# Kernel tuning notes

Measured on AMD Instinct MI355X. Metric: run time of the kernel, lower is better.

The kernel has to match this reference:

```python
import jax, jax.numpy as jnp
import numpy as np

B, N, D, C, H = 32, 36, 2048, 4, 512  # batch, regions, feat dim, coord dim, fusion hidden


def setup_inputs() -> dict:
    key = jax.random.key(0)
    ks = jax.random.split(key, 8)
    w = lambda k, sh: jax.random.normal(k, sh, dtype=jnp.float32) * 0.02
    return {
        "mm": jax.random.normal(ks[0], (B, N, D), dtype=jnp.float32),
        "coords": jax.random.uniform(ks[1], (B, N, C), dtype=jnp.float32),
        # MLB fusion params for coords: z = (x@W_cl * y@W_cr) @ W_cout
        "W_cl": w(ks[2], (C, H)),
        "W_cr": w(ks[3], (C, H)),
        "W_cout": w(ks[4], (H, D)),
        # MLB fusion params for features
        "W_fl": w(ks[5], (D, H)),
        "W_fr": w(ks[6], (D, H)),
        "W_fout": w(ks[7], (H, D)),
    }


def reference(mm, coords, W_cl, W_cr, W_cout, W_fl, W_fr, W_fout):
    # Project once per region (avoids projecting inside the N*N expand).
    cl = coords @ W_cl            # [B,N,H]
    cr = coords @ W_cr            # [B,N,H]
    fl = mm @ W_fl                # [B,N,H]
    fr = mm @ W_fr                # [B,N,H]
    # All-pairs bilinear fusion: Rij = f_coord(c_i, c_j) + f_feat(m_i, m_j)
    pair_c = cl[:, :, None, :] * cr[:, None, :, :]   # [B,N,N,H]
    pair_f = fl[:, :, None, :] * fr[:, None, :, :]   # [B,N,N,H]
    Rij = (jnp.einsum('bijh,hd->bijd', pair_c, W_cout)
           + jnp.einsum('bijh,hd->bijd', pair_f, W_fout))  # [B,N,N,D]
    # agg['type'] == 'max': reduce over the right (j) region axis
    mm_new = Rij.max(axis=2)      # [B,N,D]
    # residual
    return mm_new + mm
```

## Files before the change

### kernel.cpp

```cpp
#include <hip/hip_runtime.h>


typedef __attribute__((ext_vector_type(8))) short short8;
typedef __attribute__((ext_vector_type(4))) short short4v;
typedef __attribute__((ext_vector_type(4))) float f32x4;

__device__ __forceinline__ float bf2f(unsigned short h) {
  return __uint_as_float(((unsigned int)h) << 16);
}
__device__ __forceinline__ unsigned short f2bf(float f) {
  unsigned int u = __float_as_uint(f);
  u += 0x7FFFu + ((u >> 16) & 1u);
  return (unsigned short)(u >> 16);
}
__device__ __forceinline__ void gl2lds16(const void* g, void* l) {
  __builtin_amdgcn_global_load_lds(
      (const __attribute__((address_space(1))) unsigned int*)g,
      (__attribute__((address_space(3))) unsigned int*)l, 16, 0, 0);
}

__global__ __launch_bounds__(256) void k_prep(
    const float* __restrict__ coords, const float* __restrict__ Wcl,
    const float* __restrict__ Wcr, const float* __restrict__ mm,
    const float* __restrict__ Wcout, const float* __restrict__ Wfout,
    const float* __restrict__ Wfl, const float* __restrict__ Wfr,
    unsigned short* __restrict__ Lw, unsigned short* __restrict__ Rw,
    unsigned short* __restrict__ mmb, unsigned short* __restrict__ WS,
    unsigned short* __restrict__ WS2) {
  const int bid = blockIdx.x;
  if (bid < 2304) {
    int idx = bid * 256 + threadIdx.x;
    int row = idx >> 9, h = idx & 511;
    const float* c = coords + row * 4;
    float a0 = c[0], a1 = c[1], a2 = c[2], a3 = c[3];
    float vl = a0 * Wcl[h] + a1 * Wcl[512 + h] + a2 * Wcl[1024 + h] + a3 * Wcl[1536 + h];
    float vr = a0 * Wcr[h] + a1 * Wcr[512 + h] + a2 * Wcr[1024 + h] + a3 * Wcr[1536 + h];
    Lw[(size_t)row * 1024 + h] = f2bf(vl);
    Rw[(size_t)row * 1024 + h] = f2bf(vr);
    float4 m4 = *(const float4*)(mm + (size_t)row * 2048 + h * 4);
    short4v o;
    o[0] = (short)f2bf(m4.x); o[1] = (short)f2bf(m4.y);
    o[2] = (short)f2bf(m4.z); o[3] = (short)f2bf(m4.w);
    *(short4v*)(mmb + (size_t)row * 2048 + h * 4) = o;
  } else {
    int gi = (bid - 2304) * 256 + threadIdx.x;
    if (gi < 262144) {
      int n = gi & 15, qv = (gi >> 4) & 3, kc = (gi >> 6) & 31, g2 = gi >> 11;
      int d = g2 * 16 + n;
      int kbase = kc * 32 + qv * 8;
      const float* src = (kbase < 512) ? (Wcout + (size_t)kbase * 2048 + d)
                                       : (Wfout + (size_t)(kbase - 512) * 2048 + d);
      short8 o;
#pragma unroll
      for (int e = 0; e < 8; ++e) o[e] = (short)f2bf(src[(size_t)e * 2048]);
      *(short8*)(WS + (size_t)gi * 8) = o;
    } else {
      int gj = gi - 262144;
      int n = gj & 15, qv = (gj >> 4) & 3, kc = (gj >> 6) & 63, cg = gj >> 12;
      int col = cg * 16 + n;
      int dbase = kc * 32 + qv * 8;
      const float* src = (col < 512) ? (Wfl + (size_t)dbase * 512 + col)
                                     : (Wfr + (size_t)dbase * 512 + (col - 512));
      short8 o;
#pragma unroll
      for (int e = 0; e < 8; ++e) o[e] = (short)f2bf(src[(size_t)e * 512]);
      *(short8*)(WS2 + (size_t)gj * 8) = o;
    }
  }
}

__global__ __launch_bounds__(256) void k_proj_feat(
    const unsigned short* __restrict__ mmb, const unsigned short* __restrict__ WS2,
    unsigned short* __restrict__ Lw, unsigned short* __restrict__ Rw) {
  const int tid = threadIdx.x;
  const int lane = tid & 63, w = tid >> 6;
  const int n = lane & 15, q = lane >> 4;
  const int m0 = blockIdx.y * 16;
  const int cg = blockIdx.x * 4 + w;
  const int c0 = cg * 16;

  f32x4 acc = {0.f, 0.f, 0.f, 0.f};
#pragma unroll 4
  for (int kc = 0; kc < 64; ++kc) {
    short8 a = *(const short8*)(mmb + (size_t)(m0 + n) * 2048 + kc * 32 + q * 8);
    short8 b = *(const short8*)(WS2 + (size_t)(cg * 64 + kc) * 512 + lane * 8);
    acc = __builtin_amdgcn_mfma_f32_16x16x32_bf16(a, b, acc, 0, 0, 0);
  }
#pragma unroll
  for (int e = 0; e < 4; ++e) {
    int row = m0 + q * 4 + e;
    int col = c0 + n;
    unsigned short v = f2bf(acc[e]);
    if (col < 512) Lw[(size_t)row * 1024 + 512 + col] = v;
    else           Rw[(size_t)row * 1024 + col] = v;
  }
}

__global__ __launch_bounds__(256) void k_prod(
    const unsigned short* __restrict__ Lw, const unsigned short* __restrict__ Rw,
    unsigned short* __restrict__ Pf) {
  int idx = blockIdx.x * 256 + threadIdx.x;
  int lane = idx & 63;
  int gran = idx >> 6;
  int qg = gran / 288;
  int rem = gran - qg * 288;
  int kc = rem / 9;
  int t = rem - kc * 9;
  int n = lane & 15, q = lane >> 4;
  int k0 = kc * 32 + q * 8;
  int b = qg / 9;
  int g, j;
  if (t < 8) { g = qg * 4 + (t >> 1); j = (t & 1) * 16 + n; }
  else       { g = qg * 4 + (n >> 2); j = 32 + (n & 3); }
  short8 cl8 = *(const short8*)(Lw + (size_t)g * 1024 + k0);
  short8 cr8 = *(const short8*)(Rw + (size_t)(b * 36 + j) * 1024 + k0);
  short8 p;
#pragma unroll
  for (int e = 0; e < 8; ++e)
    p[e] = (short)f2bf(bf2f((unsigned short)cl8[e]) * bf2f((unsigned short)cr8[e]));
  *(short8*)(Pf + (size_t)idx * 8) = p;
}

__global__ __launch_bounds__(512, 2) void k_pairwise(
    const unsigned short* __restrict__ Pf, const unsigned short* __restrict__ WS,
    const float* __restrict__ mm, float* __restrict__ out) {
  __shared__ __align__(16) unsigned short lB[2][9 * 512];

  const int tid = threadIdx.x;
  const int lane = tid & 63, w = tid >> 6;
  const int n = lane & 15, q = lane >> 4;
  const int bx = blockIdx.x;
  const int dt = bx & 7, qg = bx >> 3;
  const int g0 = qg * 4;

  f32x4 acc[9][2];
#pragma unroll
  for (int t = 0; t < 9; ++t)
#pragma unroll
    for (int r = 0; r < 2; ++r) acc[t][r] = (f32x4){0.f, 0.f, 0.f, 0.f};

  const unsigned short* Abase = WS + ((size_t)(dt * 16 + w * 2) * 32) * 512 + lane * 8;
  const unsigned short* Bbase = Pf + (size_t)qg * 32 * 9 * 512;

  short8 aR[2], aN[2];
  gl2lds16(Bbase + (size_t)w * 512 + lane * 8, &lB[0][w * 512]);
  if (w == 0) gl2lds16(Bbase + (size_t)8 * 512 + lane * 8, &lB[0][8 * 512]);
  aR[0] = *(const short8*)(Abase);
  aR[1] = *(const short8*)(Abase + 32 * 512);
  __syncthreads();

#pragma unroll 2
  for (int kc = 0; kc < 32; ++kc) {
    const int buf = kc & 1;
    if (kc < 31) {
      const unsigned short* bn = Bbase + (size_t)((kc + 1) * 9) * 512 + lane * 8;
      gl2lds16(bn + (size_t)w * 512, &lB[buf ^ 1][w * 512]);
      if (w == 0) gl2lds16(bn + (size_t)8 * 512, &lB[buf ^ 1][8 * 512]);
      aN[0] = *(const short8*)(Abase + (size_t)(kc + 1) * 512);
      aN[1] = *(const short8*)(Abase + (size_t)(32 + kc + 1) * 512);
    }
    short8 bb[9];
#pragma unroll
    for (int t = 0; t < 9; ++t)
      bb[t] = *(const short8*)(&lB[buf][t * 512 + lane * 8]);
#pragma unroll
    for (int t = 0; t < 9; ++t) {
      acc[t][0] = __builtin_amdgcn_mfma_f32_16x16x32_bf16(aR[0], bb[t], acc[t][0], 0, 0, 0);
      acc[t][1] = __builtin_amdgcn_mfma_f32_16x16x32_bf16(aR[1], bb[t], acc[t][1], 0, 0, 0);
    }
    __syncthreads();
    aR[0] = aN[0];
    aR[1] = aN[1];
  }

#pragma unroll
  for (int r = 0; r < 2; ++r) {
#pragma unroll
    for (int e = 0; e < 4; ++e) {
      float vs = acc[8][r][e];
#pragma unroll
      for (int ii = 0; ii < 4; ++ii) {
        float v = fmaxf(acc[ii * 2][r][e], acc[ii * 2 + 1][r][e]);
        v = fmaxf(v, ((n >> 2) == ii) ? vs : -1e30f);
#pragma unroll
        for (int s = 1; s < 16; s <<= 1) v = fmaxf(v, __shfl_xor(v, s, 64));
        if (n == 0) {
          int d = dt * 256 + w * 32 + r * 16 + q * 4 + e;
          size_t o = (size_t)(g0 + ii) * 2048 + d;
          out[o] = v + mm[o];
        }
      }
    }
  }
}

extern "C" void kernel_launch(void* const* d_in, const int* in_sizes, int n_in,
                              void* d_out, int out_size, void* d_ws, size_t ws_size,
                              hipStream_t stream) {
  const float* mm     = (const float*)d_in[0];
  const float* coords = (const float*)d_in[1];
  const float* Wcl    = (const float*)d_in[2];
  const float* Wcr    = (const float*)d_in[3];
  const float* Wcout  = (const float*)d_in[4];
  const float* Wfl    = (const float*)d_in[5];
  const float* Wfr    = (const float*)d_in[6];
  const float* Wfout  = (const float*)d_in[7];
  float* out = (float*)d_out;

  unsigned short* Lw  = (unsigned short*)d_ws;
  unsigned short* Rw  = Lw + 1152 * 1024;
  unsigned short* WS  = Rw + 1152 * 1024;
  unsigned short* WS2 = WS + (size_t)262144 * 8;
  unsigned short* mmb = WS2 + (size_t)262144 * 8;
  unsigned short* Pf  = mmb + (size_t)1152 * 2048;

  k_prep<<<2304 + 2048, 256, 0, stream>>>(coords, Wcl, Wcr, mm, Wcout, Wfout,
                                          Wfl, Wfr, Lw, Rw, mmb, WS, WS2);
  k_proj_feat<<<dim3(16, 72), 256, 0, stream>>>(mmb, WS2, Lw, Rw);
  k_prod<<<20736, 256, 0, stream>>>(Lw, Rw, Pf);
  k_pairwise<<<2304, 512, 0, stream>>>(Pf, WS, mm, out);
}
```

Before: 341.5 us.

## Fuse pairwise product into GEMM kernel, drop materialized Pf buffer

Removes the separate k_prod kernel that wrote the full all-pairs bf16 product tensor to global memory. k_pairwise now loads the fp32 L/R projections directly, multiplies and packs them to bf16 in registers, and stores them into LDS. The K-loop is restructured to process two k-chunks per iteration with a doubled LDS buffer. Projections are now kept in fp32, so the product is rounded once instead of twice. The cost is redundant product computation across the 8 d-tile blocks, plus register-staged prefetch in place of async global-to-LDS loads.

```diff
diff --git a/kernel.cpp b/kernel.cpp
--- a/kernel.cpp
+++ b/kernel.cpp
@@ -1,22 +1,30 @@
 #include <hip/hip_runtime.h>
+#include <hip/hip_bf16.h>
 
 
 typedef __attribute__((ext_vector_type(8))) short short8;
 typedef __attribute__((ext_vector_type(4))) short short4v;
 typedef __attribute__((ext_vector_type(4))) float f32x4;
-
-__device__ __forceinline__ float bf2f(unsigned short h) {
-  return __uint_as_float(((unsigned int)h) << 16);
-}
+typedef __attribute__((ext_vector_type(8))) float f32x8;
+typedef __attribute__((ext_vector_type(4))) unsigned int u32x4;
+
 __device__ __forceinline__ unsigned short f2bf(float f) {
   unsigned int u = __float_as_uint(f);
   u += 0x7FFFu + ((u >> 16) & 1u);
   return (unsigned short)(u >> 16);
 }
-__device__ __forceinline__ void gl2lds16(const void* g, void* l) {
-  __builtin_amdgcn_global_load_lds(
-      (const __attribute__((address_space(1))) unsigned int*)g,
-      (__attribute__((address_space(3))) unsigned int*)l, 16, 0, 0);
+
+__device__ __forceinline__ u32x4 pack8(f32x8 a, f32x8 b) {
+  u32x4 o;
+#pragma unroll
+  for (int e2 = 0; e2 < 4; ++e2) {
+    __hip_bfloat162 h = __float22bfloat162_rn(
+        make_float2(a[2 * e2] * b[2 * e2], a[2 * e2 + 1] * b[2 * e2 + 1]));
+    unsigned int u;
+    __builtin_memcpy(&u, &h, sizeof(u));
+    o[e2] = u;
+  }
+  return o;
 }
 
 __global__ __launch_bounds__(256) void k_prep(
@@ -24,7 +32,7 @@
     const float* __restrict__ Wcr, const float* __restrict__ mm,
     const float* __restrict__ Wcout, const float* __restrict__ Wfout,
     const float* __restrict__ Wfl, const float* __restrict__ Wfr,
-    unsigned short* __restrict__ Lw, unsigned short* __restrict__ Rw,
+    float* __restrict__ Lw, float* __restrict__ Rw,
     unsigned short* __restrict__ mmb, unsigned short* __restrict__ WS,
     unsigned short* __restrict__ WS2) {
   const int bid = blockIdx.x;
@@ -35,8 +43,8 @@
     float a0 = c[0], a1 = c[1], a2 = c[2], a3 = c[3];
     float vl = a0 * Wcl[h] + a1 * Wcl[512 + h] + a2 * Wcl[1024 + h] + a3 * Wcl[1536 + h];
     float vr = a0 * Wcr[h] + a1 * Wcr[512 + h] + a2 * Wcr[1024 + h] + a3 * Wcr[1536 + h];
-    Lw[(size_t)row * 1024 + h] = f2bf(vl);
-    Rw[(size_t)row * 1024 + h] = f2bf(vr);
+    Lw[(size_t)row * 1024 + h] = vl;
+    Rw[(size_t)row * 1024 + h] = vr;
     float4 m4 = *(const float4*)(mm + (size_t)row * 2048 + h * 4);
     short4v o;
     o[0] = (short)f2bf(m4.x); o[1] = (short)f2bf(m4.y);
@@ -71,7 +79,7 @@
 
 __global__ __launch_bounds__(256) void k_proj_feat(
     const unsigned short* __restrict__ mmb, const unsigned short* __restrict__ WS2,
-    unsigned short* __restrict__ Lw, unsigned short* __restrict__ Rw) {
+    float* __restrict__ Lw, float* __restrict__ Rw) {
   const int tid = threadIdx.x;
   const int lane = tid & 63, w = tid >> 6;
   const int n = lane & 15, q = lane >> 4;
@@ -90,41 +98,16 @@
   for (int e = 0; e < 4; ++e) {
     int row = m0 + q * 4 + e;
     int col = c0 + n;
-    unsigned short v = f2bf(acc[e]);
-    if (col < 512) Lw[(size_t)row * 1024 + 512 + col] = v;
-    else           Rw[(size_t)row * 1024 + col] = v;
-  }
-}
-
-__global__ __launch_bounds__(256) void k_prod(
-    const unsigned short* __restrict__ Lw, const unsigned short* __restrict__ Rw,
-    unsigned short* __restrict__ Pf) {
-  int idx = blockIdx.x * 256 + threadIdx.x;
-  int lane = idx & 63;
-  int gran = idx >> 6;
-  int qg = gran / 288;
-  int rem = gran - qg * 288;
-  int kc = rem / 9;
-  int t = rem - kc * 9;
-  int n = lane & 15, q = lane >> 4;
-  int k0 = kc * 32 + q * 8;
-  int b = qg / 9;
-  int g, j;
-  if (t < 8) { g = qg * 4 + (t >> 1); j = (t & 1) * 16 + n; }
-  else       { g = qg * 4 + (n >> 2); j = 32 + (n & 3); }
-  short8 cl8 = *(const short8*)(Lw + (size_t)g * 1024 + k0);
-  short8 cr8 = *(const short8*)(Rw + (size_t)(b * 36 + j) * 1024 + k0);
-  short8 p;
-#pragma unroll
-  for (int e = 0; e < 8; ++e)
-    p[e] = (short)f2bf(bf2f((unsigned short)cl8[e]) * bf2f((unsigned short)cr8[e]));
-  *(short8*)(Pf + (size_t)idx * 8) = p;
+    if (col < 512) Lw[(size_t)row * 1024 + 512 + col] = acc[e];
+    else           Rw[(size_t)row * 1024 + col] = acc[e];
+  }
 }
 
 __global__ __launch_bounds__(512, 2) void k_pairwise(
-    const unsigned short* __restrict__ Pf, const unsigned short* __restrict__ WS,
-    const float* __restrict__ mm, float* __restrict__ out) {
-  __shared__ __align__(16) unsigned short lB[2][9 * 512];
+    const float* __restrict__ Lw, const float* __restrict__ Rw,
+    const unsigned short* __restrict__ WS, const float* __restrict__ mm,
+    float* __restrict__ out) {
+  __shared__ __align__(16) unsigned short lB[2][2 * 9 * 512];
 
   const int tid = threadIdx.x;
   const int lane = tid & 63, w = tid >> 6;
@@ -132,6 +115,19 @@
   const int bx = blockIdx.x;
   const int dt = bx & 7, qg = bx >> 3;
   const int g0 = qg * 4;
+  const int b36 = (qg / 9) * 36;
+
+  const int g_p = g0 + (w >> 1);
+  const int j_p = (w & 1) * 16 + n;
+  const int ls = w * 8 + (lane & 7);
+  const int qs = ls >> 4, ns = ls & 15;
+  const int g_s = g0 + (ns >> 2);
+  const int j_s = 32 + (ns & 3);
+
+  const float* Lp = Lw + (size_t)g_p * 1024 + q * 8;
+  const float* Rp = Rw + (size_t)(b36 + j_p) * 1024 + q * 8;
+  const float* Ls = Lw + (size_t)g_s * 1024 + qs * 8;
+  const float* Rs = Rw + (size_t)(b36 + j_s) * 1024 + qs * 8;
 
   f32x4 acc[9][2];
 #pragma unroll
@@ -140,37 +136,69 @@
     for (int r = 0; r < 2; ++r) acc[t][r] = (f32x4){0.f, 0.f, 0.f, 0.f};
 
   const unsigned short* Abase = WS + ((size_t)(dt * 16 + w * 2) * 32) * 512 + lane * 8;
-  const unsigned short* Bbase = Pf + (size_t)qg * 32 * 9 * 512;
-
-  short8 aR[2], aN[2];
-  gl2lds16(Bbase + (size_t)w * 512 + lane * 8, &lB[0][w * 512]);
-  if (w == 0) gl2lds16(Bbase + (size_t)8 * 512 + lane * 8, &lB[0][8 * 512]);
-  aR[0] = *(const short8*)(Abase);
-  aR[1] = *(const short8*)(Abase + 32 * 512);
+
+  short8 aC[2][2];
+
+#pragma unroll
+  for (int kci = 0; kci < 2; ++kci) {
+#pragma unroll
+    for (int r = 0; r < 2; ++r)
+      aC[kci][r] = *(const short8*)(Abase + (size_t)(r * 32 + kci) * 512);
+    f32x8 c0 = *(const f32x8*)(Lp + kci * 32);
+    f32x8 r0 = *(const f32x8*)(Rp + kci * 32);
+    *(u32x4*)(&lB[0][kci * 4608 + w * 512 + lane * 8]) = pack8(c0, r0);
+    if ((lane & 63) < 8) {
+      f32x8 c1 = *(const f32x8*)(Ls + kci * 32);
+      f32x8 r1 = *(const f32x8*)(Rs + kci * 32);
+      *(u32x4*)(&lB[0][kci * 4608 + 8 * 512 + ls * 8]) = pack8(c1, r1);
+    }
+  }
   __syncthreads();
 
-#pragma unroll 2
-  for (int kc = 0; kc < 32; ++kc) {
-    const int buf = kc & 1;
-    if (kc < 31) {
-      const unsigned short* bn = Bbase + (size_t)((kc + 1) * 9) * 512 + lane * 8;
-      gl2lds16(bn + (size_t)w * 512, &lB[buf ^ 1][w * 512]);
-      if (w == 0) gl2lds16(bn + (size_t)8 * 512, &lB[buf ^ 1][8 * 512]);
-      aN[0] = *(const short8*)(Abase + (size_t)(kc + 1) * 512);
-      aN[1] = *(const short8*)(Abase + (size_t)(32 + kc + 1) * 512);
-    }
-    short8 bb[9];
-#pragma unroll
-    for (int t = 0; t < 9; ++t)
-      bb[t] = *(const short8*)(&lB[buf][t * 512 + lane * 8]);
+  for (int p = 0; p < 16; ++p) {
+    const int buf = p & 1;
+    const bool pre = (p < 15);
+    f32x8 pcl[2], pcr[2], scl[2], scr[2];
+    short8 aN[2][2];
+    if (pre) {
+      const int kb = (p + 1) * 2;
+#pragma unroll
+      for (int kci = 0; kci < 2; ++kci) {
+#pragma unroll
+        for (int r = 0; r < 2; ++r)
+          aN[kci][r] = *(const short8*)(Abase + (size_t)(r * 32 + kb + kci) * 512);
+        pcl[kci] = *(const f32x8*)(Lp + (kb + kci) * 32);
+        pcr[kci] = *(const f32x8*)(Rp + (kb + kci) * 32);
+        if ((lane & 63) < 8) {
+          scl[kci] = *(const f32x8*)(Ls + (kb + kci) * 32);
+          scr[kci] = *(const f32x8*)(Rs + (kb + kci) * 32);
+        }
+      }
+    }
 #pragma unroll
     for (int t = 0; t < 9; ++t) {
-      acc[t][0] = __builtin_amdgcn_mfma_f32_16x16x32_bf16(aR[0], bb[t], acc[t][0], 0, 0, 0);
-      acc[t][1] = __builtin_amdgcn_mfma_f32_16x16x32_bf16(aR[1], bb[t], acc[t][1], 0, 0, 0);
+      short8 b0 = *(const short8*)(&lB[buf][t * 512 + lane * 8]);
+      short8 b1 = *(const short8*)(&lB[buf][4608 + t * 512 + lane * 8]);
+      acc[t][0] = __builtin_amdgcn_mfma_f32_16x16x32_bf16(aC[0][0], b0, acc[t][0], 0, 0, 0);
+      acc[t][1] = __builtin_amdgcn_mfma_f32_16x16x32_bf16(aC[0][1], b0, acc[t][1], 0, 0, 0);
+      acc[t][0] = __builtin_amdgcn_mfma_f32_16x16x32_bf16(aC[1][0], b1, acc[t][0], 0, 0, 0);
+      acc[t][1] = __builtin_amdgcn_mfma_f32_16x16x32_bf16(aC[1][1], b1, acc[t][1], 0, 0, 0);
+    }
+    if (pre) {
+#pragma unroll
+      for (int kci = 0; kci < 2; ++kci) {
+        *(u32x4*)(&lB[buf ^ 1][kci * 4608 + w * 512 + lane * 8]) = pack8(pcl[kci], pcr[kci]);
+        if ((lane & 63) < 8)
+          *(u32x4*)(&lB[buf ^ 1][kci * 4608 + 8 * 512 + ls * 8]) = pack8(scl[kci], scr[kci]);
+      }
     }
     __syncthreads();
-    aR[0] = aN[0];
-    aR[1] = aN[1];
+    if (pre) {
+#pragma unroll
+      for (int kci = 0; kci < 2; ++kci)
+#pragma unroll
+        for (int r = 0; r < 2; ++r) aC[kci][r] = aN[kci][r];
+    }
   }
 
 #pragma unroll
@@ -207,16 +235,14 @@
   const float* Wfout  = (const float*)d_in[7];
   float* out = (float*)d_out;
 
-  unsigned short* Lw  = (unsigned short*)d_ws;
-  unsigned short* Rw  = Lw + 1152 * 1024;
-  unsigned short* WS  = Rw + 1152 * 1024;
+  float* Lw = (float*)d_ws;
+  float* Rw = Lw + (size_t)1152 * 1024;
+  unsigned short* WS  = (unsigned short*)(Rw + (size_t)1152 * 1024);
   unsigned short* WS2 = WS + (size_t)262144 * 8;
   unsigned short* mmb = WS2 + (size_t)262144 * 8;
-  unsigned short* Pf  = mmb + (size_t)1152 * 2048;
 
   k_prep<<<2304 + 2048, 256, 0, stream>>>(coords, Wcl, Wcr, mm, Wcout, Wfout,
                                           Wfl, Wfr, Lw, Rw, mmb, WS, WS2);
   k_proj_feat<<<dim3(16, 72), 256, 0, stream>>>(mmb, WS2, Lw, Rw);
-  k_prod<<<20736, 256, 0, stream>>>(Lw, Rw, Pf);
-  k_pairwise<<<2304, 512, 0, stream>>>(Pf, WS, mm, out);
-}
+  k_pairwise<<<2304, 512, 0, stream>>>(Lw, Rw, WS, mm, out);
+}
```

Result: slower. 559.0 us (+63.7%).

## Fold coord bilinear branch into 16-term outer-product weight matrix

Applied to the files above, without the earlier changes.

Because the coordinate dimension is 4, the coord MLB branch (cl_i*cr_j)@W_cout is rewritten as (c_i ⊗ c_j)@Mc, where Mc is a 16x2048 matrix precomputed from W_cl, W_cr and W_cout. The K dimension of the pairwise GEMM shrinks from 1024 to 528 (512 feature terms plus one padded 32-wide chunk holding the 16 outer-product terms). Pf and WS shrink to match, which roughly halves MFMA work and memory traffic in the dominant kernels. It adds a small serial k_mc kernel (8 blocks, each looping over 512 h) and changes rounding, since Mc is formed in fp32 and then rounded to bf16.

```diff
diff --git a/kernel.cpp b/kernel.cpp
--- a/kernel.cpp
+++ b/kernel.cpp
@@ -19,24 +19,41 @@
       (__attribute__((address_space(3))) unsigned int*)l, 16, 0, 0);
 }
 
+__global__ __launch_bounds__(256) void k_mc(
+    const float* __restrict__ Wcl, const float* __restrict__ Wcr,
+    const float* __restrict__ Wcout, float* __restrict__ Mc) {
+  const int d = blockIdx.x * 256 + threadIdx.x;
+  float acc[16];
+#pragma unroll
+  for (int i = 0; i < 16; ++i) acc[i] = 0.f;
+  for (int h = 0; h < 512; ++h) {
+    float wo = Wcout[(size_t)h * 2048 + d];
+    float cl[4], cr[4];
+#pragma unroll
+    for (int a = 0; a < 4; ++a) {
+      cl[a] = Wcl[a * 512 + h];
+      cr[a] = Wcr[a * 512 + h];
+    }
+#pragma unroll
+    for (int a = 0; a < 4; ++a) {
+      float t = cl[a] * wo;
+#pragma unroll
+      for (int b = 0; b < 4; ++b) acc[a * 4 + b] += t * cr[b];
+    }
+  }
+#pragma unroll
+  for (int ab = 0; ab < 16; ++ab) Mc[(size_t)ab * 2048 + d] = acc[ab];
+}
+
 __global__ __launch_bounds__(256) void k_prep(
-    const float* __restrict__ coords, const float* __restrict__ Wcl,
-    const float* __restrict__ Wcr, const float* __restrict__ mm,
-    const float* __restrict__ Wcout, const float* __restrict__ Wfout,
-    const float* __restrict__ Wfl, const float* __restrict__ Wfr,
-    unsigned short* __restrict__ Lw, unsigned short* __restrict__ Rw,
-    unsigned short* __restrict__ mmb, unsigned short* __restrict__ WS,
-    unsigned short* __restrict__ WS2) {
+    const float* __restrict__ mm, const float* __restrict__ Wfout,
+    const float* __restrict__ Mc, const float* __restrict__ Wfl,
+    const float* __restrict__ Wfr, unsigned short* __restrict__ mmb,
+    unsigned short* __restrict__ WS, unsigned short* __restrict__ WS2) {
   const int bid = blockIdx.x;
   if (bid < 2304) {
     int idx = bid * 256 + threadIdx.x;
     int row = idx >> 9, h = idx & 511;
-    const float* c = coords + row * 4;
-    float a0 = c[0], a1 = c[1], a2 = c[2], a3 = c[3];
-    float vl = a0 * Wcl[h] + a1 * Wcl[512 + h] + a2 * Wcl[1024 + h] + a3 * Wcl[1536 + h];
-    float vr = a0 * Wcr[h] + a1 * Wcr[512 + h] + a2 * Wcr[1024 + h] + a3 * Wcr[1536 + h];
-    Lw[(size_t)row * 1024 + h] = f2bf(vl);
-    Rw[(size_t)row * 1024 + h] = f2bf(vr);
     float4 m4 = *(const float4*)(mm + (size_t)row * 2048 + h * 4);
     short4v o;
     o[0] = (short)f2bf(m4.x); o[1] = (short)f2bf(m4.y);
@@ -44,18 +61,27 @@
     *(short4v*)(mmb + (size_t)row * 2048 + h * 4) = o;
   } else {
     int gi = (bid - 2304) * 256 + threadIdx.x;
-    if (gi < 262144) {
-      int n = gi & 15, qv = (gi >> 4) & 3, kc = (gi >> 6) & 31, g2 = gi >> 11;
+    if (gi < 139264) {
+      int n = gi & 15, qv = (gi >> 4) & 3, rest = gi >> 6;
+      int kc = rest % 17, g2 = rest / 17;
       int d = g2 * 16 + n;
-      int kbase = kc * 32 + qv * 8;
-      const float* src = (kbase < 512) ? (Wcout + (size_t)kbase * 2048 + d)
-                                       : (Wfout + (size_t)(kbase - 512) * 2048 + d);
       short8 o;
-#pragma unroll
-      for (int e = 0; e < 8; ++e) o[e] = (short)f2bf(src[(size_t)e * 2048]);
+      if (kc < 16) {
+        int kbase = kc * 32 + qv * 8;
+        const float* src = Wfout + (size_t)kbase * 2048 + d;
+#pragma unroll
+        for (int e = 0; e < 8; ++e) o[e] = (short)f2bf(src[(size_t)e * 2048]);
+      } else if (qv < 2) {
+        const float* src = Mc + (size_t)(qv * 8) * 2048 + d;
+#pragma unroll
+        for (int e = 0; e < 8; ++e) o[e] = (short)f2bf(src[(size_t)e * 2048]);
+      } else {
+#pragma unroll
+        for (int e = 0; e < 8; ++e) o[e] = 0;
+      }
       *(short8*)(WS + (size_t)gi * 8) = o;
     } else {
-      int gj = gi - 262144;
+      int gj = gi - 139264;
       int n = gj & 15, qv = (gj >> 4) & 3, kc = (gj >> 6) & 63, cg = gj >> 12;
       int col = cg * 16 + n;
       int dbase = kc * 32 + qv * 8;
@@ -71,7 +97,7 @@
 
 __global__ __launch_bounds__(256) void k_proj_feat(
     const unsigned short* __restrict__ mmb, const unsigned short* __restrict__ WS2,
-    unsigned short* __restrict__ Lw, unsigned short* __restrict__ Rw) {
+    unsigned short* __restrict__ Fl, unsigned short* __restrict__ Fr) {
   const int tid = threadIdx.x;
   const int lane = tid & 63, w = tid >> 6;
   const int n = lane & 15, q = lane >> 4;
@@ -91,33 +117,50 @@
     int row = m0 + q * 4 + e;
     int col = c0 + n;
     unsigned short v = f2bf(acc[e]);
-    if (col < 512) Lw[(size_t)row * 1024 + 512 + col] = v;
-    else           Rw[(size_t)row * 1024 + col] = v;
+    if (col < 512) Fl[(size_t)row * 512 + col] = v;
+    else           Fr[(size_t)row * 512 + (col - 512)] = v;
   }
 }
 
 __global__ __launch_bounds__(256) void k_prod(
-    const unsigned short* __restrict__ Lw, const unsigned short* __restrict__ Rw,
-    unsigned short* __restrict__ Pf) {
+    const unsigned short* __restrict__ Fl, const unsigned short* __restrict__ Fr,
+    const float* __restrict__ coords, unsigned short* __restrict__ Pf) {
   int idx = blockIdx.x * 256 + threadIdx.x;
   int lane = idx & 63;
   int gran = idx >> 6;
-  int qg = gran / 288;
-  int rem = gran - qg * 288;
+  int qg = gran / 153;
+  int rem = gran - qg * 153;
   int kc = rem / 9;
   int t = rem - kc * 9;
   int n = lane & 15, q = lane >> 4;
-  int k0 = kc * 32 + q * 8;
   int b = qg / 9;
   int g, j;
   if (t < 8) { g = qg * 4 + (t >> 1); j = (t & 1) * 16 + n; }
   else       { g = qg * 4 + (n >> 2); j = 32 + (n & 3); }
-  short8 cl8 = *(const short8*)(Lw + (size_t)g * 1024 + k0);
-  short8 cr8 = *(const short8*)(Rw + (size_t)(b * 36 + j) * 1024 + k0);
+  int rowj = b * 36 + j;
   short8 p;
-#pragma unroll
-  for (int e = 0; e < 8; ++e)
-    p[e] = (short)f2bf(bf2f((unsigned short)cl8[e]) * bf2f((unsigned short)cr8[e]));
+  if (kc < 16) {
+    int k0 = kc * 32 + q * 8;
+    short8 cl8 = *(const short8*)(Fl + (size_t)g * 512 + k0);
+    short8 cr8 = *(const short8*)(Fr + (size_t)rowj * 512 + k0);
+#pragma unroll
+    for (int e = 0; e < 8; ++e)
+      p[e] = (short)f2bf(bf2f((unsigned short)cl8[e]) * bf2f((unsigned short)cr8[e]));
+  } else if (q < 2) {
+    float4 ci = *(const float4*)(coords + (size_t)g * 4);
+    float4 cj = *(const float4*)(coords + (size_t)rowj * 4);
+#pragma unroll
+    for (int e = 0; e < 8; ++e) {
+      int a = q * 2 + (e >> 2);
+      float ca = (a == 0) ? ci.x : (a == 1) ? ci.y : (a == 2) ? ci.z : ci.w;
+      float cb = ((e & 3) == 0) ? cj.x : ((e & 3) == 1) ? cj.y
+               : ((e & 3) == 2) ? cj.z : cj.w;
+      p[e] = (short)f2bf(ca * cb);
+    }
+  } else {
+#pragma unroll
+    for (int e = 0; e < 8; ++e) p[e] = 0;
+  }
   *(short8*)(Pf + (size_t)idx * 8) = p;
 }
 
@@ -139,25 +182,25 @@
 #pragma unroll
     for (int r = 0; r < 2; ++r) acc[t][r] = (f32x4){0.f, 0.f, 0.f, 0.f};
 
-  const unsigned short* Abase = WS + ((size_t)(dt * 16 + w * 2) * 32) * 512 + lane * 8;
-  const unsigned short* Bbase = Pf + (size_t)qg * 32 * 9 * 512;
+  const unsigned short* Abase = WS + ((size_t)(dt * 16 + w * 2) * 17) * 512 + lane * 8;
+  const unsigned short* Bbase = Pf + (size_t)qg * 17 * 9 * 512;
 
   short8 aR[2], aN[2];
   gl2lds16(Bbase + (size_t)w * 512 + lane * 8, &lB[0][w * 512]);
   if (w == 0) gl2lds16(Bbase + (size_t)8 * 512 + lane * 8, &lB[0][8 * 512]);
   aR[0] = *(const short8*)(Abase);
-  aR[1] = *(const short8*)(Abase + 32 * 512);
+  aR[1] = *(const short8*)(Abase + 17 * 512);
   __syncthreads();
 
 #pragma unroll 2
-  for (int kc = 0; kc < 32; ++kc) {
+  for (int kc = 0; kc < 17; ++kc) {
     const int buf = kc & 1;
-    if (kc < 31) {
+    if (kc < 16) {
       const unsigned short* bn = Bbase + (size_t)((kc + 1) * 9) * 512 + lane * 8;
       gl2lds16(bn + (size_t)w * 512, &lB[buf ^ 1][w * 512]);
       if (w == 0) gl2lds16(bn + (size_t)8 * 512, &lB[buf ^ 1][8 * 512]);
       aN[0] = *(const short8*)(Abase + (size_t)(kc + 1) * 512);
-      aN[1] = *(const short8*)(Abase + (size_t)(32 + kc + 1) * 512);
+      aN[1] = *(const short8*)(Abase + (size_t)(17 + kc + 1) * 512);
     }
     short8 bb[9];
 #pragma unroll
@@ -207,16 +250,17 @@
   const float* Wfout  = (const float*)d_in[7];
   float* out = (float*)d_out;
 
-  unsigned short* Lw  = (unsigned short*)d_ws;
-  unsigned short* Rw  = Lw + 1152 * 1024;
-  unsigned short* WS  = Rw + 1152 * 1024;
-  unsigned short* WS2 = WS + (size_t)262144 * 8;
+  float* Mc = (float*)d_ws;
+  unsigned short* Fl  = (unsigned short*)(Mc + 16 * 2048);
+  unsigned short* Fr  = Fl + (size_t)1152 * 512;
+  unsigned short* WS  = Fr + (size_t)1152 * 512;
+  unsigned short* WS2 = WS + (size_t)139264 * 8;
   unsigned short* mmb = WS2 + (size_t)262144 * 8;
   unsigned short* Pf  = mmb + (size_t)1152 * 2048;
 
-  k_prep<<<2304 + 2048, 256, 0, stream>>>(coords, Wcl, Wcr, mm, Wcout, Wfout,
-                                          Wfl, Wfr, Lw, Rw, mmb, WS, WS2);
-  k_proj_feat<<<dim3(16, 72), 256, 0, stream>>>(mmb, WS2, Lw, Rw);
-  k_prod<<<20736, 256, 0, stream>>>(Lw, Rw, Pf);
+  k_mc<<<8, 256, 0, stream>>>(Wcl, Wcr, Wcout, Mc);
+  k_prep<<<2304 + 1568, 256, 0, stream>>>(mm, Wfout, Mc, Wfl, Wfr, mmb, WS, WS2);
+  k_proj_feat<<<dim3(16, 72), 256, 0, stream>>>(mmb, WS2, Fl, Fr);
+  k_prod<<<11016, 256, 0, stream>>>(Fl, Fr, coords, Pf);
   k_pairwise<<<2304, 512, 0, stream>>>(Pf, WS, mm, out);
 }
```

After: 384.2 us. 12.5% more time.
